# Optimization experiments

Hardware: AMD Instinct MI355X
Metric: run time of the kernel (lower is better)

The kernel has to match this reference:

```python
import jax, jax.numpy as jnp
import numpy as np

WIN_SIZE = 11
WIN_SIGMA = 1.5
DATA_RANGE = 1.0
K1, K2 = 0.01, 0.03


def _gauss_1d(size, sigma):
    coords = np.arange(size, dtype=np.float64) - size // 2
    g = np.exp(-(coords ** 2) / (2.0 * sigma ** 2))
    g = g / g.sum()
    return jnp.asarray(g, dtype=jnp.float32)


def _gaussian_filter(x, win1d):
    # x: (N, C, H, W); separable depthwise gaussian blur, VALID padding
    C = x.shape[1]
    dn = ('NCHW', 'OIHW', 'NCHW')
    kh = jnp.tile(win1d.reshape(1, 1, -1, 1), (C, 1, 1, 1))
    kw = jnp.tile(win1d.reshape(1, 1, 1, -1), (C, 1, 1, 1))
    x = jax.lax.conv_general_dilated(x, kh, (1, 1), 'VALID', dimension_numbers=dn, feature_group_count=C)
    x = jax.lax.conv_general_dilated(x, kw, (1, 1), 'VALID', dimension_numbers=dn, feature_group_count=C)
    return x


def setup_inputs() -> dict:
    key = jax.random.key(0)
    k1, k2 = jax.random.split(key)
    shape = (32, 1, 512, 512)
    y_pred = jax.random.uniform(k1, shape, dtype=jnp.float32)
    y_true = jax.random.uniform(k2, shape, dtype=jnp.float32)
    return {"y_pred": y_pred, "y_true": y_true}


def reference(y_pred, y_true):
    # SSIMLoss.forward: 1 - ssim(y_true, y_pred, data_range=1.0, size_average=True)
    C1 = (K1 * DATA_RANGE) ** 2
    C2 = (K2 * DATA_RANGE) ** 2
    win = _gauss_1d(WIN_SIZE, WIN_SIGMA)

    X, Y = y_true, y_pred
    mu1 = _gaussian_filter(X, win)
    mu2 = _gaussian_filter(Y, win)
    sigma1_sq = _gaussian_filter(X * X, win) - mu1 * mu1
    sigma2_sq = _gaussian_filter(Y * Y, win) - mu2 * mu2
    sigma12 = _gaussian_filter(X * Y, win) - mu1 * mu2

    cs_map = (2.0 * sigma12 + C2) / (sigma1_sq + sigma2_sq + C2)
    ssim_map = ((2.0 * mu1 * mu2 + C1) / (mu1 * mu1 + mu2 * mu2 + C1)) * cs_map
    # size_average=True -> mean over everything
    return 1.0 - jnp.mean(ssim_map)
```

## Files before the change

kernel.cpp:

```cpp
#include <hip/hip_runtime.h>
#include <cmath>

#define IMG      512
#define OUT      502
#define TW       64
#define TH       32
#define IW       74
#define PITCH    76
#define MOFF     (TH * PITCH)
#define NTHREADS 256
#define TILES_X  8
#define TILES_Y  16
#define NIMG     32
#define NBLOCKS  (TILES_X * TILES_Y * NIMG)

struct GaussW { float w[11]; };

__global__ __launch_bounds__(NTHREADS, 3)
void ssim_tile_kernel(const float* __restrict__ ypred,
                      const float* __restrict__ ytrue,
                      float* __restrict__ partials,
                      GaussW gw)
{
    __shared__ __align__(16) float sV[5 * MOFF];
    __shared__ float wsum[4];

    const int t     = threadIdx.x;
    const int tileX = blockIdx.x, tileY = blockIdx.y, img = blockIdx.z;
    const int ox0 = (tileX == TILES_X - 1) ? (OUT - TW) : tileX * TW;
    const int oy0 = (tileY == TILES_Y - 1) ? (OUT - TH) : tileY * TH;

    const size_t imgoff = (size_t)img * (IMG * IMG);
    const float* __restrict__ Xp = ytrue + imgoff;
    const float* __restrict__ Yp = ypred + imgoff;

    if (t < IW * 3) {
        const int c  = t % IW;
        const int g  = t / IW;
        const int r0 = g * 11;

        const float* __restrict__ Xc = Xp + (size_t)(oy0 + r0) * IMG + (ox0 + c);
        const float* __restrict__ Yc = Yp + (size_t)(oy0 + r0) * IMG + (ox0 + c);

        float acc[5][11];
        #pragma unroll
        for (int m = 0; m < 5; ++m)
            #pragma unroll
            for (int j = 0; j < 11; ++j) acc[m][j] = 0.f;

        #pragma unroll
        for (int k = 0; k < 20; ++k) {
            const float x = Xc[k * IMG];
            const float y = Yc[k * IMG];
            const float xx = x * x, yy = y * y, xy = x * y;
            #pragma unroll
            for (int j = 0; j < 11; ++j) {
                if (k - j >= 0 && k - j <= 10) {
                    const float w = gw.w[k - j];
                    acc[0][j] += w * x;
                    acc[1][j] += w * y;
                    acc[2][j] += w * xx;
                    acc[3][j] += w * yy;
                    acc[4][j] += w * xy;
                }
            }
        }
        if (g < 2) {
            const float x = Xc[20 * IMG];
            const float y = Yc[20 * IMG];
            const float w = gw.w[10];
            acc[0][10] += w * x;
            acc[1][10] += w * y;
            acc[2][10] += w * (x * x);
            acc[3][10] += w * (y * y);
            acc[4][10] += w * (x * y);
        }

        const int o0 = r0 * PITCH + c;
        #pragma unroll
        for (int j = 0; j < 10; ++j) {
            const int o = o0 + j * PITCH;
            sV[0 * MOFF + o] = acc[0][j];
            sV[1 * MOFF + o] = acc[1][j];
            sV[2 * MOFF + o] = acc[2][j];
            sV[3 * MOFF + o] = acc[3][j];
            sV[4 * MOFF + o] = acc[4][j];
        }
        if (g < 2) {
            const int o = o0 + 10 * PITCH;
            sV[0 * MOFF + o] = acc[0][10];
            sV[1 * MOFF + o] = acc[1][10];
            sV[2 * MOFF + o] = acc[2][10];
            sV[3 * MOFF + o] = acc[3][10];
            sV[4 * MOFF + o] = acc[4][10];
        }
    }
    __syncthreads();

    const float C1 = 0.0001f;
    const float C2 = 0.0009f;

    const int row  = t & 31;
    const int seg  = t >> 5;
    const int base = row * PITCH + seg * 8;

    float res[5][8];
    #pragma unroll
    for (int m = 0; m < 5; ++m) {
        const float4 q0 = *reinterpret_cast<const float4*>(&sV[base + m * MOFF +  0]);
        const float4 q1 = *reinterpret_cast<const float4*>(&sV[base + m * MOFF +  4]);
        const float4 q2 = *reinterpret_cast<const float4*>(&sV[base + m * MOFF +  8]);
        const float4 q3 = *reinterpret_cast<const float4*>(&sV[base + m * MOFF + 12]);
        const float4 q4 = *reinterpret_cast<const float4*>(&sV[base + m * MOFF + 16]);
        const float win[20] = { q0.x, q0.y, q0.z, q0.w,
                                q1.x, q1.y, q1.z, q1.w,
                                q2.x, q2.y, q2.z, q2.w,
                                q3.x, q3.y, q3.z, q3.w,
                                q4.x, q4.y, q4.z, q4.w };
        #pragma unroll
        for (int c = 0; c < 8; ++c) {
            float r = 0.f;
            #pragma unroll
            for (int k = 0; k < 11; ++k) r += gw.w[k] * win[c + k];
            res[m][c] = r;
        }
    }

    const int  oy     = oy0 + row;
    const bool rowown = (oy >= tileY * TH);
    float lsum = 0.f;

    #pragma unroll
    for (int c = 0; c < 8; ++c) {
        const int  ox  = ox0 + seg * 8 + c;
        const bool own = rowown && (ox >= tileX * TW);
        const float mu1 = res[0][c], mu2 = res[1][c];
        const float s1  = res[2][c] - mu1 * mu1;
        const float s2  = res[3][c] - mu2 * mu2;
        const float s12 = res[4][c] - mu1 * mu2;
        const float num = (2.f * mu1 * mu2 + C1) * (2.f * s12 + C2);
        const float den = (mu1 * mu1 + mu2 * mu2 + C1) * (s1 + s2 + C2);
        const float ssim = num / den;
        lsum += own ? ssim : 0.f;
    }

    #pragma unroll
    for (int off = 32; off > 0; off >>= 1) lsum += __shfl_down(lsum, off, 64);
    if ((t & 63) == 0) wsum[t >> 6] = lsum;
    __syncthreads();
    if (t == 0) {
        const float b = wsum[0] + wsum[1] + wsum[2] + wsum[3];
        partials[((size_t)img * TILES_Y + tileY) * TILES_X + tileX] = b;
    }
}

__global__ void ssim_reduce_kernel(const float* __restrict__ partials,
                                   float* __restrict__ out)
{
    __shared__ double ws[4];
    const int t = threadIdx.x;
    double s = 0.0;
    for (int i = t; i < NBLOCKS; i += 256) s += (double)partials[i];
    #pragma unroll
    for (int off = 32; off > 0; off >>= 1) s += __shfl_down(s, off, 64);
    if ((t & 63) == 0) ws[t >> 6] = s;
    __syncthreads();
    if (t == 0) {
        const double total = ws[0] + ws[1] + ws[2] + ws[3];
        const double mean  = total / ((double)OUT * (double)OUT * (double)NIMG);
        out[0] = (float)(1.0 - mean);
    }
}

extern "C" void kernel_launch(void* const* d_in, const int* in_sizes, int n_in,
                              void* d_out, int out_size, void* d_ws, size_t ws_size,
                              hipStream_t stream)
{
    const float* ypred = (const float*)d_in[0];
    const float* ytrue = (const float*)d_in[1];
    float* out      = (float*)d_out;
    float* partials = (float*)d_ws;

    GaussW gw;
    double g[11], sum = 0.0;
    for (int i = 0; i < 11; ++i) {
        const double c = (double)i - 5.0;
        g[i] = std::exp(-(c * c) / (2.0 * 1.5 * 1.5));
        sum += g[i];
    }
    for (int i = 0; i < 11; ++i) gw.w[i] = (float)(g[i] / sum);

    dim3 grid(TILES_X, TILES_Y, NIMG);
    ssim_tile_kernel<<<grid, NTHREADS, 0, stream>>>(ypred, ytrue, partials, gw);
    ssim_reduce_kernel<<<1, 256, 0, stream>>>(partials, out);
}
```

Before: 127.4 us.

## Merge x² and y² blurs into one channel and use fast reciprocal

Blurs the sum x²+y² as a single channel instead of x² and y² separately, because SSIM only needs sigma1+sigma2. This cuts the blurred channels from five to four, reducing accumulator registers, LDS footprint and horizontal-pass work, and the launch bound is raised to 4 blocks per SM. The ssim division becomes a multiply by the hardware approximate reciprocal, and the load addressing switches to a 32-bit offset. The risks are a small loss of precision from the fast reciprocal and possible register spills under the tighter occupancy bound.

```diff
diff --git a/kernel.cpp b/kernel.cpp
--- a/kernel.cpp
+++ b/kernel.cpp
@@ -16,13 +16,13 @@
 
 struct GaussW { float w[11]; };
 
-__global__ __launch_bounds__(NTHREADS, 3)
+__global__ __launch_bounds__(NTHREADS, 4)
 void ssim_tile_kernel(const float* __restrict__ ypred,
                       const float* __restrict__ ytrue,
                       float* __restrict__ partials,
                       GaussW gw)
 {
-    __shared__ __align__(16) float sV[5 * MOFF];
+    __shared__ __align__(16) float sV[4 * MOFF];
     __shared__ float wsum[4];
 
     const int t     = threadIdx.x;
@@ -39,41 +39,40 @@
         const int g  = t / IW;
         const int r0 = g * 11;
 
-        const float* __restrict__ Xc = Xp + (size_t)(oy0 + r0) * IMG + (ox0 + c);
-        const float* __restrict__ Yc = Yp + (size_t)(oy0 + r0) * IMG + (ox0 + c);
+        unsigned off = (unsigned)((oy0 + r0) * IMG + (ox0 + c));
 
-        float acc[5][11];
+        float acc[4][11];
         #pragma unroll
-        for (int m = 0; m < 5; ++m)
+        for (int m = 0; m < 4; ++m)
             #pragma unroll
             for (int j = 0; j < 11; ++j) acc[m][j] = 0.f;
 
         #pragma unroll
         for (int k = 0; k < 20; ++k) {
-            const float x = Xc[k * IMG];
-            const float y = Yc[k * IMG];
-            const float xx = x * x, yy = y * y, xy = x * y;
+            const float x = Xp[off];
+            const float y = Yp[off];
+            off += IMG;
+            const float s = __builtin_fmaf(y, y, x * x);
+            const float p = x * y;
             #pragma unroll
             for (int j = 0; j < 11; ++j) {
                 if (k - j >= 0 && k - j <= 10) {
                     const float w = gw.w[k - j];
                     acc[0][j] += w * x;
                     acc[1][j] += w * y;
-                    acc[2][j] += w * xx;
-                    acc[3][j] += w * yy;
-                    acc[4][j] += w * xy;
+                    acc[2][j] += w * s;
+                    acc[3][j] += w * p;
                 }
             }
         }
         if (g < 2) {
-            const float x = Xc[20 * IMG];
-            const float y = Yc[20 * IMG];
+            const float x = Xp[off];
+            const float y = Yp[off];
             const float w = gw.w[10];
             acc[0][10] += w * x;
             acc[1][10] += w * y;
-            acc[2][10] += w * (x * x);
-            acc[3][10] += w * (y * y);
-            acc[4][10] += w * (x * y);
+            acc[2][10] += w * __builtin_fmaf(y, y, x * x);
+            acc[3][10] += w * (x * y);
         }
 
         const int o0 = r0 * PITCH + c;
@@ -84,7 +83,6 @@
             sV[1 * MOFF + o] = acc[1][j];
             sV[2 * MOFF + o] = acc[2][j];
             sV[3 * MOFF + o] = acc[3][j];
-            sV[4 * MOFF + o] = acc[4][j];
         }
         if (g < 2) {
             const int o = o0 + 10 * PITCH;
@@ -92,7 +90,6 @@
             sV[1 * MOFF + o] = acc[1][10];
             sV[2 * MOFF + o] = acc[2][10];
             sV[3 * MOFF + o] = acc[3][10];
-            sV[4 * MOFF + o] = acc[4][10];
         }
     }
     __syncthreads();
@@ -104,9 +101,9 @@
     const int seg  = t >> 5;
     const int base = row * PITCH + seg * 8;
 
-    float res[5][8];
+    float res[4][8];
     #pragma unroll
-    for (int m = 0; m < 5; ++m) {
+    for (int m = 0; m < 4; ++m) {
         const float4 q0 = *reinterpret_cast<const float4*>(&sV[base + m * MOFF +  0]);
         const float4 q1 = *reinterpret_cast<const float4*>(&sV[base + m * MOFF +  4]);
         const float4 q2 = *reinterpret_cast<const float4*>(&sV[base + m * MOFF +  8]);
@@ -135,12 +132,13 @@
         const int  ox  = ox0 + seg * 8 + c;
         const bool own = rowown && (ox >= tileX * TW);
         const float mu1 = res[0][c], mu2 = res[1][c];
-        const float s1  = res[2][c] - mu1 * mu1;
-        const float s2  = res[3][c] - mu2 * mu2;
-        const float s12 = res[4][c] - mu1 * mu2;
-        const float num = (2.f * mu1 * mu2 + C1) * (2.f * s12 + C2);
-        const float den = (mu1 * mu1 + mu2 * mu2 + C1) * (s1 + s2 + C2);
-        const float ssim = num / den;
+        const float b3  = res[2][c];
+        const float b4  = res[3][c];
+        const float P   = mu1 * mu2;
+        const float S   = __builtin_fmaf(mu1, mu1, mu2 * mu2);
+        const float num = __builtin_fmaf(2.f, P, C1) * __builtin_fmaf(2.f, b4 - P, C2);
+        const float den = (S + C1) * ((b3 + C2) - S);
+        const float ssim = num * __builtin_amdgcn_rcpf(den);
         lsum += own ? ssim : 0.f;
     }
 
```

After: 116.4 us. 8.6% less time.
